# Kernel tuning notes

Hardware: AMD Instinct MI355X
Metric: run time of the kernel (lower is better)

## Reference

```python
import jax, jax.numpy as jnp
import numpy as np

B, N, DEG, D, ED = 4, 4096, 16, 128, 256
E = N * DEG
BN_EPS = 1e-5


def _l2norm(x):
    # F.normalize(p=2, dim=-1) with eps clamp
    n = jnp.linalg.norm(x, axis=-1, keepdims=True)
    return x / jnp.maximum(n, 1e-12)


def _bn_eval(x, g, b, m, v):
    return (x - m) * jax.lax.rsqrt(v + BN_EPS) * g + b


def setup_inputs() -> dict:
    key = jax.random.key(0)
    ks = jax.random.split(key, 8)
    node_feat = jax.random.normal(ks[0], (B, N, D), jnp.float32)
    # fixed-degree edge list, grouped by source node
    src_grp = jnp.broadcast_to(jnp.arange(N, dtype=jnp.int32)[:, None], (N, DEG))
    step = (N - 1) // DEG  # distinct targets per source
    tgt_grp = (src_grp + 1 + (jnp.arange(DEG, dtype=jnp.int32) * step)[None, :]) % N
    src_idx = jnp.broadcast_to(src_grp.reshape(1, E), (B, E)).astype(jnp.int32)
    tgt_grp_b = (tgt_grp[None] + jnp.arange(B, dtype=jnp.int32)[:, None, None]) % N
    tgt_idx = tgt_grp_b.reshape(B, E).astype(jnp.int32)

    def lin(k, fi, fo):
        return jax.random.normal(k, (fi, fo), jnp.float32) * (2.0 / fi) ** 0.5

    kk = jax.random.split(ks[1], 5)
    return {
        "node_feat": node_feat, "src_idx": src_idx, "tgt_idx": tgt_idx,
        "Wa1": lin(kk[0], 2 * D, D), "ba1": jnp.zeros((D,), jnp.float32),
        "Wa2": lin(kk[1], D, D), "ba2": jnp.zeros((D,), jnp.float32),
        "W1": lin(kk[2], 3 * D, ED), "b1": jnp.zeros((ED,), jnp.float32),
        "g1": jnp.ones((ED,), jnp.float32), "be1": jnp.zeros((ED,), jnp.float32),
        "m1": jnp.zeros((ED,), jnp.float32), "v1": jnp.ones((ED,), jnp.float32),
        "W2": lin(kk[3], ED, ED // 2), "b2": jnp.zeros((ED // 2,), jnp.float32),
        "g2": jnp.ones((ED // 2,), jnp.float32), "be2": jnp.zeros((ED // 2,), jnp.float32),
        "m2": jnp.zeros((ED // 2,), jnp.float32), "v2": jnp.ones((ED // 2,), jnp.float32),
        "W3": lin(kk[4], ED // 2, 1), "b3": jnp.zeros((1,), jnp.float32),
        "min_edges_per_node": 4,
    }


def reference(node_feat, src_idx, tgt_idx, Wa1, ba1, Wa2, ba2,
              W1, b1, g1, be1, m1, v1, W2, b2, g2, be2, m2, v2,
              W3, b3, min_edges_per_node):
    # gather endpoint features: [B, E, D]
    gather = jax.vmap(lambda nf, idx: nf[idx])
    sf = _l2norm(gather(node_feat, src_idx))
    tf = _l2norm(gather(node_feat, tgt_idx))
    feat_diff = jnp.abs(sf - tf)
    raw = jnp.concatenate([sf, tf], axis=-1)                      # [B,E,2D]
    att = jax.nn.softmax(jnp.maximum(raw @ Wa1 + ba1, 0.0) @ Wa2 + ba2, axis=-1)
    edge_feats = jnp.concatenate([sf, tf, feat_diff * att], axis=-1)  # [B,E,3D]
    h = jnp.maximum(_bn_eval(edge_feats @ W1 + b1, g1, be1, m1, v1), 0.0)
    h = jnp.maximum(_bn_eval(h @ W2 + b2, g2, be2, m2, v2), 0.0)
    logits = (h @ W3 + b3)[..., 0]                                # [B,E]
    scores = jax.nn.sigmoid(logits)

    # eval-mode 50th-percentile thresholding
    thr_idx = min(E * 50 // 100, E - 1)
    thr = jnp.sort(scores, axis=-1)[:, E - 1 - thr_idx]           # desc index thr_idx
    above = scores >= thr[:, None]
    # per-source repair of min_edges_per_node (edges grouped by src)
    grp_s = scores.reshape(B, N, DEG)
    grp_a = above.reshape(B, N, DEG)
    active = grp_a.sum(-1)
    me = jnp.int32(min_edges_per_node)
    need = jnp.where(active < me, jnp.minimum(me - active, DEG), 0)
    rank = jnp.argsort(jnp.argsort(-grp_s, axis=-1), axis=-1)     # 0 = highest score
    keep = grp_a | (rank < need[:, :, None])
    final = jnp.where(keep, grp_s, 0.0).reshape(B, E)

    # scatter to dense edge-weight matrix [B,N,N]
    b_ix = jnp.arange(B, dtype=jnp.int32)[:, None]
    edge_weights = jnp.zeros((B, N, N), final.dtype).at[b_ix, src_idx, tgt_idx].set(final)
    return edge_weights
```

## Files before the change

kernel.cpp:

```cpp
#include <hip/hip_runtime.h>
#include <math.h>

#define BB 4
#define NN 4096
#define DEGQ 16
#define DDIM 128
#define EDIM 256
#define EE (NN*DEGQ)
#define STR 68
#define STR4 17

#define WS_XN     0
#define WS_UVPQ   (WS_XN + BB*NN*DDIM)
#define WS_SCORES (WS_UVPQ + (size_t)BB*NN*768)
#define WS_THR    (WS_SCORES + (size_t)BB*EE)
#define WS_SELP   (WS_THR + 8)
#define WS_SELR   (WS_SELP + 4)
#define WS_GHIST  (WS_SELR + 4)
#define WS_BN     (WS_GHIST + 1024)

__global__ void k_norm(const float* __restrict__ nf, float* __restrict__ xn) {
    int wave = (blockIdx.x * blockDim.x + threadIdx.x) >> 6;
    int lane = threadIdx.x & 63;
    if (wave >= BB * NN) return;
    const float* row = nf + (size_t)wave * DDIM;
    float2 v = *(const float2*)(row + 2 * lane);
    float ss = v.x * v.x + v.y * v.y;
#pragma unroll
    for (int d = 32; d; d >>= 1) ss += __shfl_xor(ss, d, 64);
    float n = fmaxf(sqrtf(ss), 1e-12f);
    float inv = 1.0f / n;
    float2 o; o.x = v.x * inv; o.y = v.y * inv;
    *(float2*)(xn + (size_t)wave * DDIM + 2 * lane) = o;
}

__global__ void k_prep(const float* g1, const float* be1, const float* m1, const float* v1,
                       const float* g2, const float* be2, const float* m2, const float* v2,
                       float* bn, unsigned* ghist, unsigned* selp, int* selr) {
    int c = threadIdx.x;
    ghist[c] = 0u; ghist[256 + c] = 0u; ghist[512 + c] = 0u; ghist[768 + c] = 0u;
    if (c < 4) { selp[c] = 0u; selr[c] = EE / 2 - 1; }
    if (c < 256) {
        float s = g1[c] / sqrtf(v1[c] + 1e-5f);
        bn[c] = s; bn[256 + c] = be1[c] - m1[c] * s;
    }
    if (c < 128) {
        float s = g2[c] / sqrtf(v2[c] + 1e-5f);
        bn[512 + c] = s; bn[640 + c] = be2[c] - m2[c] * s;
    }
}

__global__ void k_uvpq(const float* __restrict__ xn, const float* __restrict__ Wa1,
                       const float* __restrict__ W1, float* __restrict__ uvpq) {
    int chunk = blockIdx.y;
    const float* wbase; int wstride; int ocol;
    switch (chunk) {
        case 0: wbase = Wa1;                 wstride = 128; ocol = 0;   break;
        case 1: wbase = Wa1 + 128 * 128;     wstride = 128; ocol = 128; break;
        case 2: wbase = W1;                  wstride = 256; ocol = 256; break;
        case 3: wbase = W1 + 128;            wstride = 256; ocol = 384; break;
        case 4: wbase = W1 + 128 * 256;      wstride = 256; ocol = 512; break;
        default: wbase = W1 + 128 * 256 + 128; wstride = 256; ocol = 640; break;
    }
    int wv = threadIdx.x >> 6, lane = threadIdx.x & 63;
    int nodebase = blockIdx.x * 32 + wv * 8;
    const float* xrow[8];
#pragma unroll
    for (int j = 0; j < 8; ++j) xrow[j] = xn + (size_t)(nodebase + j) * DDIM;
    float acc0[8] = {}, acc1[8] = {};
#pragma unroll 4
    for (int k = 0; k < 128; ++k) {
        float w0 = wbase[k * wstride + lane];
        float w1 = wbase[k * wstride + 64 + lane];
#pragma unroll
        for (int j = 0; j < 8; ++j) {
            float a = xrow[j][k];
            acc0[j] = fmaf(a, w0, acc0[j]);
            acc1[j] = fmaf(a, w1, acc1[j]);
        }
    }
#pragma unroll
    for (int j = 0; j < 8; ++j) {
        float* orow = uvpq + (size_t)(nodebase + j) * 768 + ocol;
        orow[lane] = acc0[j];
        orow[64 + lane] = acc1[j];
    }
}

__global__ __launch_bounds__(512) void
k_edge(const float* __restrict__ xn, const float* __restrict__ uvpq,
       const float* __restrict__ Wa2, const float* __restrict__ ba1,
       const float* __restrict__ ba2, const float* __restrict__ W1,
       const float* __restrict__ b1, const float* __restrict__ W2,
       const float* __restrict__ b2, const float* __restrict__ W3,
       const float* __restrict__ b3, const int* __restrict__ src,
       const int* __restrict__ tgt, const float* __restrict__ bn,
       float* __restrict__ scores) {
    __shared__ float smem[256 * STR];
    __shared__ int ssrc[64], stgt[64];
    int tid = threadIdx.x;
    int b = blockIdx.y;
    int T0 = blockIdx.x * 64;
    if (tid < 64) {
        ssrc[tid] = src[(size_t)b * EE + T0 + tid];
        stgt[tid] = tgt[(size_t)b * EE + T0 + tid];
    }
    __syncthreads();

    const float* uv = uvpq + (size_t)b * NN * 768;
    const float* xb = xn + (size_t)b * NN * DDIM;
    int wv = tid >> 6, lane = tid & 63;
    int ebase = 8 * wv;
    const float4* A4 = (const float4*)smem;

    {
        int k0 = 16 * wv;
        const float* urow = uv + (size_t)ssrc[lane] * 768 + k0;
        const float* vrow = uv + (size_t)stgt[lane] * 768 + 128 + k0;
#pragma unroll
        for (int it = 0; it < 16; ++it) {
            float h = urow[it] + vrow[it] + ba1[k0 + it];
            smem[(k0 + it) * STR + lane] = fmaxf(h, 0.0f);
        }
    }
    __syncthreads();

    {
        float acc0[8] = {}, acc1[8] = {};
        const float* wa = Wa2 + lane;
#pragma unroll 4
        for (int k = 0; k < 128; ++k) {
            float w0 = wa[k * 128];
            float w1 = wa[k * 128 + 64];
            float4 hA = A4[k * STR4 + 2 * wv];
            float4 hB = A4[k * STR4 + 2 * wv + 1];
            acc0[0] = fmaf(hA.x, w0, acc0[0]); acc1[0] = fmaf(hA.x, w1, acc1[0]);
            acc0[1] = fmaf(hA.y, w0, acc0[1]); acc1[1] = fmaf(hA.y, w1, acc1[1]);
            acc0[2] = fmaf(hA.z, w0, acc0[2]); acc1[2] = fmaf(hA.z, w1, acc1[2]);
            acc0[3] = fmaf(hA.w, w0, acc0[3]); acc1[3] = fmaf(hA.w, w1, acc1[3]);
            acc0[4] = fmaf(hB.x, w0, acc0[4]); acc1[4] = fmaf(hB.x, w1, acc1[4]);
            acc0[5] = fmaf(hB.y, w0, acc0[5]); acc1[5] = fmaf(hB.y, w1, acc1[5]);
            acc0[6] = fmaf(hB.z, w0, acc0[6]); acc1[6] = fmaf(hB.z, w1, acc1[6]);
            acc0[7] = fmaf(hB.w, w0, acc0[7]); acc1[7] = fmaf(hB.w, w1, acc1[7]);
        }
        float bb0 = ba2[lane], bb1 = ba2[64 + lane];
#pragma unroll
        for (int j = 0; j < 8; ++j) {
            float a0 = acc0[j] + bb0, a1 = acc1[j] + bb1;
            float m = fmaxf(a0, a1);
#pragma unroll
            for (int d = 32; d; d >>= 1) m = fmaxf(m, __shfl_xor(m, d, 64));
            float p0 = expf(a0 - m), p1 = expf(a1 - m);
            float s = p0 + p1;
#pragma unroll
            for (int d = 32; d; d >>= 1) s += __shfl_xor(s, d, 64);
            float inv = 1.0f / s;
            int e = ebase + j;
            const float* xs = xb + (size_t)ssrc[e] * DDIM;
            const float* xt = xb + (size_t)stgt[e] * DDIM;
            float d0 = fabsf(xs[lane] - xt[lane]);
            float d1 = fabsf(xs[64 + lane] - xt[64 + lane]);
            smem[128 * STR + lane * STR + e] = d0 * p0 * inv;
            smem[128 * STR + (64 + lane) * STR + e] = d1 * p1 * inv;
        }
    }
    __syncthreads();

    float acc2[8][4] = {};
    {
        const float* wc = W1 + 256 * 256 + lane;
#pragma unroll 2
        for (int k = 0; k < 128; ++k) {
            float w0 = wc[k * 256];
            float w1 = wc[k * 256 + 64];
            float w2 = wc[k * 256 + 128];
            float w3 = wc[k * 256 + 192];
            float4 gA = A4[128 * STR4 + k * STR4 + 2 * wv];
            float4 gB = A4[128 * STR4 + k * STR4 + 2 * wv + 1];
            acc2[0][0] = fmaf(gA.x, w0, acc2[0][0]); acc2[0][1] = fmaf(gA.x, w1, acc2[0][1]);
            acc2[0][2] = fmaf(gA.x, w2, acc2[0][2]); acc2[0][3] = fmaf(gA.x, w3, acc2[0][3]);
            acc2[1][0] = fmaf(gA.y, w0, acc2[1][0]); acc2[1][1] = fmaf(gA.y, w1, acc2[1][1]);
            acc2[1][2] = fmaf(gA.y, w2, acc2[1][2]); acc2[1][3] = fmaf(gA.y, w3, acc2[1][3]);
            acc2[2][0] = fmaf(gA.z, w0, acc2[2][0]); acc2[2][1] = fmaf(gA.z, w1, acc2[2][1]);
            acc2[2][2] = fmaf(gA.z, w2, acc2[2][2]); acc2[2][3] = fmaf(gA.z, w3, acc2[2][3]);
            acc2[3][0] = fmaf(gA.w, w0, acc2[3][0]); acc2[3][1] = fmaf(gA.w, w1, acc2[3][1]);
            acc2[3][2] = fmaf(gA.w, w2, acc2[3][2]); acc2[3][3] = fmaf(gA.w, w3, acc2[3][3]);
            acc2[4][0] = fmaf(gB.x, w0, acc2[4][0]); acc2[4][1] = fmaf(gB.x, w1, acc2[4][1]);
            acc2[4][2] = fmaf(gB.x, w2, acc2[4][2]); acc2[4][3] = fmaf(gB.x, w3, acc2[4][3]);
            acc2[5][0] = fmaf(gB.y, w0, acc2[5][0]); acc2[5][1] = fmaf(gB.y, w1, acc2[5][1]);
            acc2[5][2] = fmaf(gB.y, w2, acc2[5][2]); acc2[5][3] = fmaf(gB.y, w3, acc2[5][3]);
            acc2[6][0] = fmaf(gB.z, w0, acc2[6][0]); acc2[6][1] = fmaf(gB.z, w1, acc2[6][1]);
            acc2[6][2] = fmaf(gB.z, w2, acc2[6][2]); acc2[6][3] = fmaf(gB.z, w3, acc2[6][3]);
            acc2[7][0] = fmaf(gB.w, w0, acc2[7][0]); acc2[7][1] = fmaf(gB.w, w1, acc2[7][1]);
            acc2[7][2] = fmaf(gB.w, w2, acc2[7][2]); acc2[7][3] = fmaf(gB.w, w3, acc2[7][3]);
        }
    }
    float s1v[4], t1v[4], b1v[4];
#pragma unroll
    for (int i = 0; i < 4; ++i) {
        int c = lane + 64 * i;
        s1v[i] = bn[c]; t1v[i] = bn[256 + c]; b1v[i] = b1[c];
    }
    __syncthreads();
#pragma unroll
    for (int j = 0; j < 8; ++j) {
        int e = ebase + j;
        const float* pr = uv + (size_t)ssrc[e] * 768 + 256;
        const float* qr = uv + (size_t)stgt[e] * 768 + 512;
#pragma unroll
        for (int i = 0; i < 4; ++i) {
            int c = lane + 64 * i;
            float y = acc2[j][i] + pr[c] + qr[c] + b1v[i];
            smem[c * STR + e] = fmaxf(fmaf(y, s1v[i], t1v[i]), 0.0f);
        }
    }
    __syncthreads();

    {
        float acc30[8] = {}, acc31[8] = {};
        const float* w2p = W2 + lane;
#pragma unroll 4
        for (int k = 0; k < 256; ++k) {
            float w0 = w2p[k * 128];
            float w1 = w2p[k * 128 + 64];
            float4 hA = A4[k * STR4 + 2 * wv];
            float4 hB = A4[k * STR4 + 2 * wv + 1];
            acc30[0] = fmaf(hA.x, w0, acc30[0]); acc31[0] = fmaf(hA.x, w1, acc31[0]);
            acc30[1] = fmaf(hA.y, w0, acc30[1]); acc31[1] = fmaf(hA.y, w1, acc31[1]);
            acc30[2] = fmaf(hA.z, w0, acc30[2]); acc31[2] = fmaf(hA.z, w1, acc31[2]);
            acc30[3] = fmaf(hA.w, w0, acc30[3]); acc31[3] = fmaf(hA.w, w1, acc31[3]);
            acc30[4] = fmaf(hB.x, w0, acc30[4]); acc31[4] = fmaf(hB.x, w1, acc31[4]);
            acc30[5] = fmaf(hB.y, w0, acc30[5]); acc31[5] = fmaf(hB.y, w1, acc31[5]);
            acc30[6] = fmaf(hB.z, w0, acc30[6]); acc31[6] = fmaf(hB.z, w1, acc31[6]);
            acc30[7] = fmaf(hB.w, w0, acc30[7]); acc31[7] = fmaf(hB.w, w1, acc31[7]);
        }
        float s2a = bn[512 + lane], t2a = bn[640 + lane];
        float s2b = bn[512 + 64 + lane], t2b = bn[640 + 64 + lane];
        float b2a = b2[lane], b2b = b2[64 + lane];
        float w3a = W3[lane], w3b = W3[64 + lane];
        float b3v = b3[0];
#pragma unroll
        for (int j = 0; j < 8; ++j) {
            float h0 = fmaxf(fmaf(acc30[j] + b2a, s2a, t2a), 0.0f);
            float h1 = fmaxf(fmaf(acc31[j] + b2b, s2b, t2b), 0.0f);
            float lp = h0 * w3a + h1 * w3b;
#pragma unroll
            for (int d = 32; d; d >>= 1) lp += __shfl_xor(lp, d, 64);
            float sc = 1.0f / (1.0f + expf(-(lp + b3v)));
            if (lane == j) scores[(size_t)b * EE + T0 + ebase + j] = sc;
        }
    }
}

__global__ void k_hist(const float* __restrict__ scores, const unsigned* __restrict__ selp,
                       unsigned* __restrict__ ghist, int pass) {
    __shared__ unsigned h[256];
    int b = blockIdx.y;
    h[threadIdx.x] = 0u;
    __syncthreads();
    unsigned pref = selp[b];
    unsigned mask = (pass == 3) ? 0u : (0xFFFFFFFFu << ((pass + 1) * 8));
    const unsigned* sb = (const unsigned*)(scores + (size_t)b * EE);
    int base = blockIdx.x * 2048;
    for (int i = base + threadIdx.x; i < base + 2048; i += 256) {
        unsigned u = sb[i];
        if ((u & mask) == pref) atomicAdd(&h[(u >> (pass * 8)) & 255], 1u);
    }
    __syncthreads();
    unsigned v = h[threadIdx.x];
    if (v) atomicAdd(&ghist[b * 256 + threadIdx.x], v);
}

__global__ void k_pick(unsigned* __restrict__ ghist, unsigned* __restrict__ selp,
                       int* __restrict__ selr, float* __restrict__ thr, int pass) {
    __shared__ unsigned sh[256];
    int b = blockIdx.x;
    unsigned* gh = ghist + b * 256;
    sh[threadIdx.x] = gh[threadIdx.x];
    __syncthreads();
    if (threadIdx.x == 0) {
        unsigned r = (unsigned)selr[b], cum = 0;
        for (int x = 0; x < 256; ++x) {
            unsigned c = sh[x];
            if (cum + c > r) {
                selp[b] |= (unsigned)x << (pass * 8);
                selr[b] = (int)(r - cum);
                break;
            }
            cum += c;
        }
        if (pass == 0) thr[b] = __uint_as_float(selp[b]);
    }
    __syncthreads();
    gh[threadIdx.x] = 0u;
}

__global__ void k_scatter(const float* __restrict__ scores, const float* __restrict__ thr,
                          const int* __restrict__ src, const int* __restrict__ tgt,
                          const int* __restrict__ mep, float* __restrict__ out) {
    int gid = blockIdx.x * 256 + threadIdx.x;
    int b = gid >> 16;
    int lane = threadIdx.x & 63;
    int j = lane & 15;
    float s = scores[gid];
    float t = thr[b];
    bool above = (s >= t);
    unsigned long long bal = __ballot(above);
    int sub = lane >> 4;
    unsigned int mask16 = (unsigned int)((bal >> (sub * 16)) & 0xFFFFull);
    int active = __popc(mask16);
    int rank = 0;
#pragma unroll
    for (int j2 = 0; j2 < 16; ++j2) {
        float sv = __shfl(s, (lane & 48) + j2, 64);
        rank += (sv > s || (sv == s && j2 < j)) ? 1 : 0;
    }
    int me = *mep;
    int need = (active < me) ? min(me - active, DEGQ) : 0;
    bool keep = above || (rank < need);
    float wgt = keep ? s : 0.0f;
    out[(size_t)b * NN * NN + (size_t)src[gid] * NN + tgt[gid]] = wgt;
}

extern "C" void kernel_launch(void* const* d_in, const int* in_sizes, int n_in,
                              void* d_out, int out_size, void* d_ws, size_t ws_size,
                              hipStream_t stream) {
    const float* nf  = (const float*)d_in[0];
    const int*   src = (const int*)d_in[1];
    const int*   tgt = (const int*)d_in[2];
    const float* Wa1 = (const float*)d_in[3];
    const float* ba1 = (const float*)d_in[4];
    const float* Wa2 = (const float*)d_in[5];
    const float* ba2 = (const float*)d_in[6];
    const float* W1  = (const float*)d_in[7];
    const float* b1  = (const float*)d_in[8];
    const float* g1  = (const float*)d_in[9];
    const float* be1 = (const float*)d_in[10];
    const float* m1  = (const float*)d_in[11];
    const float* v1  = (const float*)d_in[12];
    const float* W2  = (const float*)d_in[13];
    const float* b2  = (const float*)d_in[14];
    const float* g2  = (const float*)d_in[15];
    const float* be2 = (const float*)d_in[16];
    const float* m2  = (const float*)d_in[17];
    const float* v2  = (const float*)d_in[18];
    const float* W3  = (const float*)d_in[19];
    const float* b3  = (const float*)d_in[20];
    const int*   mep = (const int*)d_in[21];

    float* ws = (float*)d_ws;
    float*    xn     = ws + WS_XN;
    float*    uvpq   = ws + WS_UVPQ;
    float*    scores = ws + WS_SCORES;
    float*    thrb   = ws + WS_THR;
    unsigned* selp   = (unsigned*)(ws + WS_SELP);
    int*      selr   = (int*)(ws + WS_SELR);
    unsigned* ghist  = (unsigned*)(ws + WS_GHIST);
    float*    bn     = ws + WS_BN;
    float*    out    = (float*)d_out;

    hipMemsetAsync(d_out, 0, (size_t)out_size * sizeof(float), stream);
    k_prep<<<1, 256, 0, stream>>>(g1, be1, m1, v1, g2, be2, m2, v2, bn, ghist, selp, selr);
    k_norm<<<(BB * NN) / 4, 256, 0, stream>>>(nf, xn);
    k_uvpq<<<dim3((BB * NN) / 32, 6), 256, 0, stream>>>(xn, Wa1, W1, uvpq);
    k_edge<<<dim3(EE / 64, BB), 512, 0, stream>>>(xn, uvpq, Wa2, ba1, ba2, W1, b1,
                                                  W2, b2, W3, b3, src, tgt, bn, scores);
    for (int pass = 3; pass >= 0; --pass) {
        k_hist<<<dim3(32, BB), 256, 0, stream>>>(scores, selp, ghist, pass);
        k_pick<<<BB, 256, 0, stream>>>(ghist, selp, selr, thrb, pass);
    }
    k_scatter<<<(BB * EE) / 256, 256, 0, stream>>>(scores, thrb, src, tgt, mep, out);
}
```

Baseline: 844.9 us.

## Remap edge MLP so lanes own edges and waves own output columns

Restructures k_edge so each lane handles one edge and each wave computes a 16-column slice of every layer. Weights are read at wave-uniform addresses (scalar or broadcast loads) and activations come from conflict-free LDS rows. Cross-lane shuffle reductions for softmax and the final dot product become per-lane LDS reductions over columns. It also shrinks LDS use and asks for 4 waves-per-EU occupancy, which risks register spills given the 64-entry temporary arrays.

```diff
diff --git a/kernel.cpp b/kernel.cpp
--- a/kernel.cpp
+++ b/kernel.cpp
@@ -7,8 +7,6 @@
 #define DDIM 128
 #define EDIM 256
 #define EE (NN*DEGQ)
-#define STR 68
-#define STR4 17
 
 #define WS_XN     0
 #define WS_UVPQ   (WS_XN + BB*NN*DDIM)
@@ -87,7 +85,7 @@
     }
 }
 
-__global__ __launch_bounds__(512) void
+__global__ __launch_bounds__(512, 4) void
 k_edge(const float* __restrict__ xn, const float* __restrict__ uvpq,
        const float* __restrict__ Wa2, const float* __restrict__ ba1,
        const float* __restrict__ ba2, const float* __restrict__ W1,
@@ -96,159 +94,186 @@
        const float* __restrict__ b3, const int* __restrict__ src,
        const int* __restrict__ tgt, const float* __restrict__ bn,
        float* __restrict__ scores) {
-    __shared__ float smem[256 * STR];
-    __shared__ int ssrc[64], stgt[64];
+    __shared__ float r1[128 * 64];
+    __shared__ float r2[128 * 64];
     int tid = threadIdx.x;
+    int lane = tid & 63;
+    int wvs = __builtin_amdgcn_readfirstlane(tid >> 6);
     int b = blockIdx.y;
     int T0 = blockIdx.x * 64;
-    if (tid < 64) {
-        ssrc[tid] = src[(size_t)b * EE + T0 + tid];
-        stgt[tid] = tgt[(size_t)b * EE + T0 + tid];
-    }
-    __syncthreads();
-
+    int se = src[(size_t)b * EE + T0 + lane];
+    int te = tgt[(size_t)b * EE + T0 + lane];
     const float* uv = uvpq + (size_t)b * NN * 768;
     const float* xb = xn + (size_t)b * NN * DDIM;
-    int wv = tid >> 6, lane = tid & 63;
-    int ebase = 8 * wv;
-    const float4* A4 = (const float4*)smem;
-
-    {
-        int k0 = 16 * wv;
-        const float* urow = uv + (size_t)ssrc[lane] * 768 + k0;
-        const float* vrow = uv + (size_t)stgt[lane] * 768 + 128 + k0;
-#pragma unroll
-        for (int it = 0; it < 16; ++it) {
-            float h = urow[it] + vrow[it] + ba1[k0 + it];
-            smem[(k0 + it) * STR + lane] = fmaxf(h, 0.0f);
-        }
-    }
-    __syncthreads();
-
-    {
-        float acc0[8] = {}, acc1[8] = {};
-        const float* wa = Wa2 + lane;
-#pragma unroll 4
+    const float* up = uv + (size_t)se * 768;
+    const float* vp = uv + (size_t)te * 768 + 128;
+    int cb = wvs * 16;
+
+    {
+        const float4* u4 = (const float4*)(up + cb);
+        const float4* v4 = (const float4*)(vp + cb);
+#pragma unroll
+        for (int q = 0; q < 4; ++q) {
+            float4 uu = u4[q], vv = v4[q];
+            float4 bb = *(const float4*)(ba1 + cb + 4 * q);
+            r1[(cb + 4 * q + 0) * 64 + lane] = fmaxf(uu.x + vv.x + bb.x, 0.0f);
+            r1[(cb + 4 * q + 1) * 64 + lane] = fmaxf(uu.y + vv.y + bb.y, 0.0f);
+            r1[(cb + 4 * q + 2) * 64 + lane] = fmaxf(uu.z + vv.z + bb.z, 0.0f);
+            r1[(cb + 4 * q + 3) * 64 + lane] = fmaxf(uu.w + vv.w + bb.w, 0.0f);
+        }
+    }
+    __syncthreads();
+
+    {
+        float acc[16] = {};
+#pragma unroll 2
         for (int k = 0; k < 128; ++k) {
-            float w0 = wa[k * 128];
-            float w1 = wa[k * 128 + 64];
-            float4 hA = A4[k * STR4 + 2 * wv];
-            float4 hB = A4[k * STR4 + 2 * wv + 1];
-            acc0[0] = fmaf(hA.x, w0, acc0[0]); acc1[0] = fmaf(hA.x, w1, acc1[0]);
-            acc0[1] = fmaf(hA.y, w0, acc0[1]); acc1[1] = fmaf(hA.y, w1, acc1[1]);
-            acc0[2] = fmaf(hA.z, w0, acc0[2]); acc1[2] = fmaf(hA.z, w1, acc1[2]);
-            acc0[3] = fmaf(hA.w, w0, acc0[3]); acc1[3] = fmaf(hA.w, w1, acc1[3]);
-            acc0[4] = fmaf(hB.x, w0, acc0[4]); acc1[4] = fmaf(hB.x, w1, acc1[4]);
-            acc0[5] = fmaf(hB.y, w0, acc0[5]); acc1[5] = fmaf(hB.y, w1, acc1[5]);
-            acc0[6] = fmaf(hB.z, w0, acc0[6]); acc1[6] = fmaf(hB.z, w1, acc1[6]);
-            acc0[7] = fmaf(hB.w, w0, acc0[7]); acc1[7] = fmaf(hB.w, w1, acc1[7]);
-        }
-        float bb0 = ba2[lane], bb1 = ba2[64 + lane];
-#pragma unroll
-        for (int j = 0; j < 8; ++j) {
-            float a0 = acc0[j] + bb0, a1 = acc1[j] + bb1;
-            float m = fmaxf(a0, a1);
-#pragma unroll
-            for (int d = 32; d; d >>= 1) m = fmaxf(m, __shfl_xor(m, d, 64));
-            float p0 = expf(a0 - m), p1 = expf(a1 - m);
-            float s = p0 + p1;
-#pragma unroll
-            for (int d = 32; d; d >>= 1) s += __shfl_xor(s, d, 64);
-            float inv = 1.0f / s;
-            int e = ebase + j;
-            const float* xs = xb + (size_t)ssrc[e] * DDIM;
-            const float* xt = xb + (size_t)stgt[e] * DDIM;
-            float d0 = fabsf(xs[lane] - xt[lane]);
-            float d1 = fabsf(xs[64 + lane] - xt[64 + lane]);
-            smem[128 * STR + lane * STR + e] = d0 * p0 * inv;
-            smem[128 * STR + (64 + lane) * STR + e] = d1 * p1 * inv;
-        }
-    }
-    __syncthreads();
-
-    float acc2[8][4] = {};
-    {
-        const float* wc = W1 + 256 * 256 + lane;
+            float h = r1[k * 64 + lane];
+            const float* wr = Wa2 + k * 128 + cb;
+#pragma unroll
+            for (int i = 0; i < 16; ++i) acc[i] = fmaf(h, wr[i], acc[i]);
+        }
+#pragma unroll
+        for (int i = 0; i < 16; ++i) r2[(cb + i) * 64 + lane] = acc[i] + ba2[cb + i];
+    }
+    __syncthreads();
+
+    float m, inv;
+    {
+        float mm[64];
+#pragma unroll
+        for (int c = 0; c < 64; ++c)
+            mm[c] = fmaxf(r2[c * 64 + lane], r2[(c + 64) * 64 + lane]);
+#pragma unroll
+        for (int d = 32; d; d >>= 1)
+#pragma unroll
+            for (int c = 0; c < d; ++c) mm[c] = fmaxf(mm[c], mm[c + d]);
+        m = mm[0];
+        float z[64];
+#pragma unroll
+        for (int c = 0; c < 64; ++c)
+            z[c] = expf(r2[c * 64 + lane] - m) + expf(r2[(c + 64) * 64 + lane] - m);
+#pragma unroll
+        for (int d = 32; d; d >>= 1)
+#pragma unroll
+            for (int c = 0; c < d; ++c) z[c] = z[c] + z[c + d];
+        inv = 1.0f / z[0];
+    }
+    {
+        const float4* xs4 = (const float4*)(xb + (size_t)se * DDIM + cb);
+        const float4* xt4 = (const float4*)(xb + (size_t)te * DDIM + cb);
+#pragma unroll
+        for (int q = 0; q < 4; ++q) {
+            float4 xs = xs4[q], xt = xt4[q];
+            float dv[4] = {fabsf(xs.x - xt.x), fabsf(xs.y - xt.y),
+                           fabsf(xs.z - xt.z), fabsf(xs.w - xt.w)};
+#pragma unroll
+            for (int r = 0; r < 4; ++r) {
+                int c = cb + 4 * q + r;
+                float p = expf(r2[c * 64 + lane] - m);
+                r1[c * 64 + lane] = dv[r] * p * inv;
+            }
+        }
+    }
+    __syncthreads();
+
+    const float* W1c = W1 + 256 * 256;
+    const float* pr = uv + (size_t)se * 768 + 256;
+    const float* qr = uv + (size_t)te * 768 + 512;
+
+    {
+        float acc[16] = {};
 #pragma unroll 2
         for (int k = 0; k < 128; ++k) {
-            float w0 = wc[k * 256];
-            float w1 = wc[k * 256 + 64];
-            float w2 = wc[k * 256 + 128];
-            float w3 = wc[k * 256 + 192];
-            float4 gA = A4[128 * STR4 + k * STR4 + 2 * wv];
-            float4 gB = A4[128 * STR4 + k * STR4 + 2 * wv + 1];
-            acc2[0][0] = fmaf(gA.x, w0, acc2[0][0]); acc2[0][1] = fmaf(gA.x, w1, acc2[0][1]);
-            acc2[0][2] = fmaf(gA.x, w2, acc2[0][2]); acc2[0][3] = fmaf(gA.x, w3, acc2[0][3]);
-            acc2[1][0] = fmaf(gA.y, w0, acc2[1][0]); acc2[1][1] = fmaf(gA.y, w1, acc2[1][1]);
-            acc2[1][2] = fmaf(gA.y, w2, acc2[1][2]); acc2[1][3] = fmaf(gA.y, w3, acc2[1][3]);
-            acc2[2][0] = fmaf(gA.z, w0, acc2[2][0]); acc2[2][1] = fmaf(gA.z, w1, acc2[2][1]);
-            acc2[2][2] = fmaf(gA.z, w2, acc2[2][2]); acc2[2][3] = fmaf(gA.z, w3, acc2[2][3]);
-            acc2[3][0] = fmaf(gA.w, w0, acc2[3][0]); acc2[3][1] = fmaf(gA.w, w1, acc2[3][1]);
-            acc2[3][2] = fmaf(gA.w, w2, acc2[3][2]); acc2[3][3] = fmaf(gA.w, w3, acc2[3][3]);
-            acc2[4][0] = fmaf(gB.x, w0, acc2[4][0]); acc2[4][1] = fmaf(gB.x, w1, acc2[4][1]);
-            acc2[4][2] = fmaf(gB.x, w2, acc2[4][2]); acc2[4][3] = fmaf(gB.x, w3, acc2[4][3]);
-            acc2[5][0] = fmaf(gB.y, w0, acc2[5][0]); acc2[5][1] = fmaf(gB.y, w1, acc2[5][1]);
-            acc2[5][2] = fmaf(gB.y, w2, acc2[5][2]); acc2[5][3] = fmaf(gB.y, w3, acc2[5][3]);
-            acc2[6][0] = fmaf(gB.z, w0, acc2[6][0]); acc2[6][1] = fmaf(gB.z, w1, acc2[6][1]);
-            acc2[6][2] = fmaf(gB.z, w2, acc2[6][2]); acc2[6][3] = fmaf(gB.z, w3, acc2[6][3]);
-            acc2[7][0] = fmaf(gB.w, w0, acc2[7][0]); acc2[7][1] = fmaf(gB.w, w1, acc2[7][1]);
-            acc2[7][2] = fmaf(gB.w, w2, acc2[7][2]); acc2[7][3] = fmaf(gB.w, w3, acc2[7][3]);
-        }
-    }
-    float s1v[4], t1v[4], b1v[4];
-#pragma unroll
-    for (int i = 0; i < 4; ++i) {
-        int c = lane + 64 * i;
-        s1v[i] = bn[c]; t1v[i] = bn[256 + c]; b1v[i] = b1[c];
-    }
-    __syncthreads();
-#pragma unroll
-    for (int j = 0; j < 8; ++j) {
-        int e = ebase + j;
-        const float* pr = uv + (size_t)ssrc[e] * 768 + 256;
-        const float* qr = uv + (size_t)stgt[e] * 768 + 512;
-#pragma unroll
-        for (int i = 0; i < 4; ++i) {
-            int c = lane + 64 * i;
-            float y = acc2[j][i] + pr[c] + qr[c] + b1v[i];
-            smem[c * STR + e] = fmaxf(fmaf(y, s1v[i], t1v[i]), 0.0f);
-        }
-    }
-    __syncthreads();
-
-    {
-        float acc30[8] = {}, acc31[8] = {};
-        const float* w2p = W2 + lane;
-#pragma unroll 4
-        for (int k = 0; k < 256; ++k) {
-            float w0 = w2p[k * 128];
-            float w1 = w2p[k * 128 + 64];
-            float4 hA = A4[k * STR4 + 2 * wv];
-            float4 hB = A4[k * STR4 + 2 * wv + 1];
-            acc30[0] = fmaf(hA.x, w0, acc30[0]); acc31[0] = fmaf(hA.x, w1, acc31[0]);
-            acc30[1] = fmaf(hA.y, w0, acc30[1]); acc31[1] = fmaf(hA.y, w1, acc31[1]);
-            acc30[2] = fmaf(hA.z, w0, acc30[2]); acc31[2] = fmaf(hA.z, w1, acc31[2]);
-            acc30[3] = fmaf(hA.w, w0, acc30[3]); acc31[3] = fmaf(hA.w, w1, acc31[3]);
-            acc30[4] = fmaf(hB.x, w0, acc30[4]); acc31[4] = fmaf(hB.x, w1, acc31[4]);
-            acc30[5] = fmaf(hB.y, w0, acc30[5]); acc31[5] = fmaf(hB.y, w1, acc31[5]);
-            acc30[6] = fmaf(hB.z, w0, acc30[6]); acc31[6] = fmaf(hB.z, w1, acc31[6]);
-            acc30[7] = fmaf(hB.w, w0, acc30[7]); acc31[7] = fmaf(hB.w, w1, acc31[7]);
-        }
-        float s2a = bn[512 + lane], t2a = bn[640 + lane];
-        float s2b = bn[512 + 64 + lane], t2b = bn[640 + 64 + lane];
-        float b2a = b2[lane], b2b = b2[64 + lane];
-        float w3a = W3[lane], w3b = W3[64 + lane];
-        float b3v = b3[0];
-#pragma unroll
-        for (int j = 0; j < 8; ++j) {
-            float h0 = fmaxf(fmaf(acc30[j] + b2a, s2a, t2a), 0.0f);
-            float h1 = fmaxf(fmaf(acc31[j] + b2b, s2b, t2b), 0.0f);
-            float lp = h0 * w3a + h1 * w3b;
-#pragma unroll
-            for (int d = 32; d; d >>= 1) lp += __shfl_xor(lp, d, 64);
-            float sc = 1.0f / (1.0f + expf(-(lp + b3v)));
-            if (lane == j) scores[(size_t)b * EE + T0 + ebase + j] = sc;
-        }
+            float g = r1[k * 64 + lane];
+            const float* wr = W1c + k * 256 + cb;
+#pragma unroll
+            for (int i = 0; i < 16; ++i) acc[i] = fmaf(g, wr[i], acc[i]);
+        }
+        float4 p4[4], q4[4];
+#pragma unroll
+        for (int q = 0; q < 4; ++q) {
+            p4[q] = *(const float4*)(pr + cb + 4 * q);
+            q4[q] = *(const float4*)(qr + cb + 4 * q);
+        }
+#pragma unroll
+        for (int i = 0; i < 16; ++i) {
+            int c = cb + i;
+            float pv = ((const float*)p4)[i], qv = ((const float*)q4)[i];
+            float y = acc[i] + pv + qv + b1[c];
+            r2[c * 64 + lane] = fmaxf(fmaf(y, bn[c], bn[256 + c]), 0.0f);
+        }
+    }
+    float h2b[16];
+    {
+        int cB = 128 + cb;
+        float acc[16] = {};
+#pragma unroll 2
+        for (int k = 0; k < 128; ++k) {
+            float g = r1[k * 64 + lane];
+            const float* wr = W1c + k * 256 + cB;
+#pragma unroll
+            for (int i = 0; i < 16; ++i) acc[i] = fmaf(g, wr[i], acc[i]);
+        }
+        float4 p4[4], q4[4];
+#pragma unroll
+        for (int q = 0; q < 4; ++q) {
+            p4[q] = *(const float4*)(pr + cB + 4 * q);
+            q4[q] = *(const float4*)(qr + cB + 4 * q);
+        }
+#pragma unroll
+        for (int i = 0; i < 16; ++i) {
+            int c = cB + i;
+            float pv = ((const float*)p4)[i], qv = ((const float*)q4)[i];
+            float y = acc[i] + pv + qv + b1[c];
+            h2b[i] = fmaxf(fmaf(y, bn[c], bn[256 + c]), 0.0f);
+        }
+    }
+    __syncthreads();
+#pragma unroll
+    for (int i = 0; i < 16; ++i) r1[(cb + i) * 64 + lane] = h2b[i];
+    __syncthreads();
+
+    {
+        float acc[16] = {};
+#pragma unroll 2
+        for (int k = 0; k < 128; ++k) {
+            float h = r2[k * 64 + lane];
+            const float* wr = W2 + k * 128 + cb;
+#pragma unroll
+            for (int i = 0; i < 16; ++i) acc[i] = fmaf(h, wr[i], acc[i]);
+        }
+#pragma unroll 2
+        for (int k = 128; k < 256; ++k) {
+            float h = r1[(k - 128) * 64 + lane];
+            const float* wr = W2 + k * 128 + cb;
+#pragma unroll
+            for (int i = 0; i < 16; ++i) acc[i] = fmaf(h, wr[i], acc[i]);
+        }
+        float prod[16];
+#pragma unroll
+        for (int i = 0; i < 16; ++i) {
+            int c = cb + i;
+            float h3 = fmaxf(fmaf(acc[i] + b2[c], bn[512 + c], bn[640 + c]), 0.0f);
+            prod[i] = h3 * W3[c];
+        }
+        __syncthreads();
+#pragma unroll
+        for (int i = 0; i < 16; ++i) r2[(cb + i) * 64 + lane] = prod[i];
+    }
+    __syncthreads();
+
+    {
+        float z[64];
+#pragma unroll
+        for (int c = 0; c < 64; ++c)
+            z[c] = r2[c * 64 + lane] + r2[(c + 64) * 64 + lane];
+#pragma unroll
+        for (int d = 32; d; d >>= 1)
+#pragma unroll
+            for (int c = 0; c < d; ++c) z[c] = z[c] + z[c + d];
+        float sc = 1.0f / (1.0f + expf(-(z[0] + b3[0])));
+        if (wvs == 0) scores[(size_t)b * EE + T0 + lane] = sc;
     }
 }
 
```

After: 1.178 ms. +39.4%, slower.
